# Optimization experiments

Hardware: AMD Instinct MI355X
Metric: run time of the kernel (lower is better)

## Reference

```python
import jax, jax.numpy as jnp
import numpy as np
import math

D_MODEL = 2048
HEADS = 16
D_K = D_MODEL // HEADS  # 128
D_FF = 2048
N = 8192
EPS = 1e-6


def _norm(x, alpha, bias):
    # torch Norm: alpha * (x - mean) / (std + eps) + bias, std uses ddof=1
    mu = jnp.mean(x, axis=-1, keepdims=True)
    sd = jnp.std(x, axis=-1, ddof=1, keepdims=True)
    return alpha * (x - mu) / (sd + EPS) + bias


def setup_inputs() -> dict:
    key = jax.random.key(0)
    ks = jax.random.split(key, 16)
    s = 0.02
    inp = {
        "q": jax.random.normal(ks[0], (N, D_MODEL), jnp.float32),
        "k": jax.random.normal(ks[1], (N, D_MODEL), jnp.float32),
        "v": jax.random.normal(ks[2], (N, D_MODEL), jnp.float32),
        # norm params (norm_1 exists in module but is unused in forward)
        "nq_a": jnp.ones((D_MODEL,), jnp.float32), "nq_b": jnp.zeros((D_MODEL,), jnp.float32),
        "nk_a": jnp.ones((D_MODEL,), jnp.float32), "nk_b": jnp.zeros((D_MODEL,), jnp.float32),
        "nv_a": jnp.ones((D_MODEL,), jnp.float32), "nv_b": jnp.zeros((D_MODEL,), jnp.float32),
        "n2_a": jnp.ones((D_MODEL,), jnp.float32), "n2_b": jnp.zeros((D_MODEL,), jnp.float32),
        # attention projections, stored [in, out]
        "Wq": jax.random.normal(ks[3], (D_MODEL, D_MODEL), jnp.float32) * s,
        "bq": jnp.zeros((D_MODEL,), jnp.float32),
        "Wk": jax.random.normal(ks[4], (D_MODEL, D_MODEL), jnp.float32) * s,
        "bk": jnp.zeros((D_MODEL,), jnp.float32),
        "Wv": jax.random.normal(ks[5], (D_MODEL, D_MODEL), jnp.float32) * s,
        "bv": jnp.zeros((D_MODEL,), jnp.float32),
        "Wo": jax.random.normal(ks[6], (D_MODEL, D_MODEL), jnp.float32) * s,
        "bo": jnp.zeros((D_MODEL,), jnp.float32),
        # FFN
        "W1": jax.random.normal(ks[7], (D_MODEL, D_FF), jnp.float32) * s,
        "b1": jnp.zeros((D_FF,), jnp.float32),
        "W2": jax.random.normal(ks[8], (D_FF, D_MODEL), jnp.float32) * s,
        "b2": jnp.zeros((D_MODEL,), jnp.float32),
    }
    return inp


def reference(q, k, v,
              nq_a, nq_b, nk_a, nk_b, nv_a, nv_b, n2_a, n2_b,
              Wq, bq, Wk, bk, Wv, bv, Wo, bo, W1, b1, W2, b2):
    x = v  # residual stream (dropout is identity at inference)
    qn = _norm(q, nq_a, nq_b)
    kn = _norm(k, nk_a, nk_b)
    vn = _norm(v, nv_a, nv_b)

    # projections -> [N, h, d_k] then transpose(1,2) -> [N, d_k, h]
    qh = (qn @ Wq + bq).reshape(N, HEADS, D_K).transpose(0, 2, 1)
    kh = (kn @ Wk + bk).reshape(N, HEADS, D_K).transpose(0, 2, 1)
    vh = (vn @ Wv + bv).reshape(N, HEADS, D_K).transpose(0, 2, 1)

    # NON-STANDARD (as-written in source): per-token [d_k, d_k] attention
    # contracting over the head axis, scaled by 1/sqrt(d_k).
    scores = jnp.einsum('nah,nbh->nab', qh, kh) / math.sqrt(D_K)  # [N, d_k, d_k]
    probs = jax.nn.softmax(scores, axis=-1)
    attn = jnp.einsum('nab,nbh->nah', probs, vh)  # [N, d_k, h]

    concat = attn.transpose(0, 2, 1).reshape(N, D_MODEL)  # [N, h*d_k]
    x = x + (concat @ Wo + bo)

    x2 = _norm(x, n2_a, n2_b)
    ff = jax.nn.relu(x2 @ W1 + b1) @ W2 + b2
    return x + ff
```

## Files before the change

### kernel.cpp

```cpp
#include <hip/hip_runtime.h>
#include <hip/hip_bf16.h>

#define DM 2048
#define NTOK 8192
#define EPS 1e-6f

typedef __attribute__((ext_vector_type(8))) short short8;
typedef __attribute__((ext_vector_type(4))) short short4v;
typedef __attribute__((ext_vector_type(4))) float f32x4;
typedef __attribute__((ext_vector_type(16))) float f32x16;
typedef __attribute__((ext_vector_type(4))) unsigned int u32x4;

typedef const __attribute__((address_space(1))) void gvoid;
typedef __attribute__((address_space(3))) void lvoid;

static __device__ __forceinline__ unsigned short f2bf(float f) {
    unsigned u = __builtin_bit_cast(unsigned, f);
    unsigned r = u + 0x7FFFu + ((u >> 16) & 1u);
    return (unsigned short)(r >> 16);
}
static __device__ __forceinline__ float bf2f(unsigned short h) {
    return __builtin_bit_cast(float, (unsigned)h << 16);
}

__global__ __launch_bounds__(256) void norm_rows(
        const float* __restrict__ in, const float* __restrict__ alpha,
        const float* __restrict__ beta, unsigned short* __restrict__ out) {
    const int row = blockIdx.x;
    const int t = threadIdx.x;
    const float* x = in + (size_t)row * DM + t * 8;
    float4 v0 = *(const float4*)(x);
    float4 v1 = *(const float4*)(x + 4);
    float s = (v0.x + v0.y) + (v0.z + v0.w) + (v1.x + v1.y) + (v1.z + v1.w);
    float ss = v0.x*v0.x + v0.y*v0.y + v0.z*v0.z + v0.w*v0.w
             + v1.x*v1.x + v1.y*v1.y + v1.z*v1.z + v1.w*v1.w;
    #pragma unroll
    for (int m = 1; m < 64; m <<= 1) {
        s  += __shfl_xor(s, m);
        ss += __shfl_xor(ss, m);
    }
    __shared__ float red[8];
    const int wv = t >> 6, ln = t & 63;
    if (ln == 0) { red[wv] = s; red[4 + wv] = ss; }
    __syncthreads();
    s  = (red[0] + red[1]) + (red[2] + red[3]);
    ss = (red[4] + red[5]) + (red[6] + red[7]);
    const float mu = s * (1.0f / DM);
    float var = (ss - s * mu) * (1.0f / (DM - 1));
    var = fmaxf(var, 0.0f);
    const float scale = 1.0f / (sqrtf(var) + EPS);
    float4 a0 = *(const float4*)(alpha + t*8);
    float4 a1 = *(const float4*)(alpha + t*8 + 4);
    float4 b0 = *(const float4*)(beta + t*8);
    float4 b1 = *(const float4*)(beta + t*8 + 4);
    short8 o;
    o[0] = (short)f2bf(a0.x * (v0.x - mu) * scale + b0.x);
    o[1] = (short)f2bf(a0.y * (v0.y - mu) * scale + b0.y);
    o[2] = (short)f2bf(a0.z * (v0.z - mu) * scale + b0.z);
    o[3] = (short)f2bf(a0.w * (v0.w - mu) * scale + b0.w);
    o[4] = (short)f2bf(a1.x * (v1.x - mu) * scale + b1.x);
    o[5] = (short)f2bf(a1.y * (v1.y - mu) * scale + b1.y);
    o[6] = (short)f2bf(a1.z * (v1.z - mu) * scale + b1.z);
    o[7] = (short)f2bf(a1.w * (v1.w - mu) * scale + b1.w);
    *(short8*)(out + (size_t)row * DM + t * 8) = o;
}

__global__ __launch_bounds__(256) void norm_rows_bf16(
        const unsigned short* __restrict__ in, const float* __restrict__ alpha,
        const float* __restrict__ beta, unsigned short* __restrict__ out) {
    const int row = blockIdx.x;
    const int t = threadIdx.x;
    short8 rv = *(const short8*)(in + (size_t)row * DM + t * 8);
    float xv[8];
    #pragma unroll
    for (int j = 0; j < 8; ++j) xv[j] = bf2f((unsigned short)rv[j]);
    float s = 0.f, ss = 0.f;
    #pragma unroll
    for (int j = 0; j < 8; ++j) { s += xv[j]; ss += xv[j]*xv[j]; }
    #pragma unroll
    for (int m = 1; m < 64; m <<= 1) {
        s  += __shfl_xor(s, m);
        ss += __shfl_xor(ss, m);
    }
    __shared__ float red[8];
    const int wv = t >> 6, ln = t & 63;
    if (ln == 0) { red[wv] = s; red[4 + wv] = ss; }
    __syncthreads();
    s  = (red[0] + red[1]) + (red[2] + red[3]);
    ss = (red[4] + red[5]) + (red[6] + red[7]);
    const float mu = s * (1.0f / DM);
    float var = (ss - s * mu) * (1.0f / (DM - 1));
    var = fmaxf(var, 0.0f);
    const float scale = 1.0f / (sqrtf(var) + EPS);
    short8 o;
    #pragma unroll
    for (int j = 0; j < 8; ++j) {
        const float av = alpha[t*8 + j], bv = beta[t*8 + j];
        o[j] = (short)f2bf(av * (xv[j] - mu) * scale + bv);
    }
    *(short8*)(out + (size_t)row * DM + t * 8) = o;
}

__global__ __launch_bounds__(256) void wtrans6(
        const float* __restrict__ Wq, const float* __restrict__ Wk,
        const float* __restrict__ Wv, const float* __restrict__ Wo,
        const float* __restrict__ W1, const float* __restrict__ W2,
        unsigned short* __restrict__ Tq, unsigned short* __restrict__ Tk,
        unsigned short* __restrict__ Tv, unsigned short* __restrict__ To,
        unsigned short* __restrict__ T1, unsigned short* __restrict__ T2,
        float isq) {
    __shared__ float tile[32][33];
    const int z = blockIdx.z;
    const float* W = z==0?Wq: z==1?Wk: z==2?Wv: z==3?Wo: z==4?W1: W2;
    unsigned short* Wt = z==0?Tq: z==1?Tk: z==2?Tv: z==3?To: z==4?T1: T2;
    const int perm = (z < 2) ? 1 : 0;
    const float ws = (z == 0) ? isq : 1.0f;
    const int bc = blockIdx.x * 32, bk = blockIdx.y * 32;
    const int t = threadIdx.x;
    const int tc = t & 31, tr = t >> 5;
    #pragma unroll
    for (int i = 0; i < 4; ++i)
        tile[tr + i*8][tc] = W[(size_t)(bk + tr + i*8) * DM + bc + tc];
    __syncthreads();
    #pragma unroll
    for (int i = 0; i < 4; ++i) {
        const int c = bc + tr + i*8;
        const int pc = perm ? ((c & 127) * 16 + (c >> 7)) : c;
        Wt[(size_t)pc * DM + bk + tc] = f2bf(tile[tc][tr + i*8] * ws);
    }
}

#define BARRIER __builtin_amdgcn_s_barrier()
#define WAIT_LGKM0 asm volatile("s_waitcnt lgkmcnt(0)" ::: "memory")
#define VMCNT(n) asm volatile("s_waitcnt vmcnt(" #n ")" ::: "memory")

template<int EPI>
__global__ __launch_bounds__(512, 2) void gemm256(
        const unsigned short* __restrict__ A, const unsigned short* __restrict__ Bt,
        const float* __restrict__ bias, const float* __restrict__ residF,
        const unsigned short* __restrict__ residB,
        float* __restrict__ outF, unsigned short* __restrict__ outB, int biasPerm,
        float bscale) {
    __shared__ __align__(16) char lds[131072];
    char* ldsA = lds;
    char* ldsB = lds + 65536;

    const int t = threadIdx.x, l = t & 63, w = t >> 6;
    const int wm = w >> 2, wn = w & 3;

    const int b = blockIdx.x;
    const int xcd = b & 7;
    const int j = b >> 3;
    const int m0 = (xcd * 4 + (j & 3)) * 256;
    const int n0 = (j >> 2) * 256;

    const int rS = t >> 3;
    const int cS = ((t & 7) ^ (rS & 7)) * 8;
    const unsigned short* aSt = A  + (size_t)(m0 + rS) * 2048 + cS;
    const unsigned short* bSt = Bt + (size_t)(n0 + rS) * 2048 + cS;
    const int ldsStW = w * 1024;

    const int aRd = wm * 16384 + (l & 15) * 128;
    const int bRd = (wn >> 1) * 16384 + (wn & 1) * 8192 + (l & 15) * 128;
    const int ch0 = (((l >> 4) + 0) ^ (l & 7)) * 16;
    const int ch1 = (((l >> 4) + 4) ^ (l & 7)) * 16;

    short8 af[8][2], bf[4][2];
    f32x4 acc[8][4] = {};

#define STG_A(buf, h, kt) do { \
    __builtin_amdgcn_global_load_lds((gvoid*)(aSt + (size_t)((h)*128)*2048 + (kt)*64), \
        (lvoid*)(ldsA + (buf)*32768 + (h)*16384 + ldsStW), 16, 0, 0); \
    __builtin_amdgcn_global_load_lds((gvoid*)(aSt + (size_t)((h)*128+64)*2048 + (kt)*64), \
        (lvoid*)(ldsA + (buf)*32768 + (h)*16384 + 8192 + ldsStW), 16, 0, 0); \
} while(0)
#define STG_B(buf, h, kt) do { \
    __builtin_amdgcn_global_load_lds((gvoid*)(bSt + (size_t)((h)*128)*2048 + (kt)*64), \
        (lvoid*)(ldsB + (buf)*32768 + (h)*16384 + ldsStW), 16, 0, 0); \
    __builtin_amdgcn_global_load_lds((gvoid*)(bSt + (size_t)((h)*128+64)*2048 + (kt)*64), \
        (lvoid*)(ldsB + (buf)*32768 + (h)*16384 + 8192 + ldsStW), 16, 0, 0); \
} while(0)
#define RD_A(buf, mh) do { \
    _Pragma("unroll") for (int ml = 0; ml < 4; ++ml) { \
        af[(mh)*4+ml][0] = *(const short8*)(ldsA + (buf)*32768 + aRd + ((mh)*4+ml)*2048 + ch0); \
        af[(mh)*4+ml][1] = *(const short8*)(ldsA + (buf)*32768 + aRd + ((mh)*4+ml)*2048 + ch1); \
    } } while(0)
#define RD_B(buf, nh) do { \
    _Pragma("unroll") for (int nl = 0; nl < 2; ++nl) { \
        bf[(nh)*2+nl][0] = *(const short8*)(ldsB + (buf)*32768 + bRd + ((nh)*2+nl)*2048 + ch0); \
        bf[(nh)*2+nl][1] = *(const short8*)(ldsB + (buf)*32768 + bRd + ((nh)*2+nl)*2048 + ch1); \
    } } while(0)
#define MM_Q(mh, nh) do { \
    _Pragma("unroll") for (int ml = 0; ml < 4; ++ml) \
    _Pragma("unroll") for (int nl = 0; nl < 2; ++nl) { \
        acc[(mh)*4+ml][(nh)*2+nl] = __builtin_amdgcn_mfma_f32_16x16x32_bf16( \
            af[(mh)*4+ml][0], bf[(nh)*2+nl][0], acc[(mh)*4+ml][(nh)*2+nl], 0, 0, 0); \
        acc[(mh)*4+ml][(nh)*2+nl] = __builtin_amdgcn_mfma_f32_16x16x32_bf16( \
            af[(mh)*4+ml][1], bf[(nh)*2+nl][1], acc[(mh)*4+ml][(nh)*2+nl], 0, 0, 0); \
    } \
} while(0)

    STG_A(0, 0, 0); STG_A(0, 1, 0);
    STG_B(0, 0, 0); STG_B(0, 1, 0);
    STG_A(1, 0, 1); STG_A(1, 1, 1);
    VMCNT(4);
    BARRIER;

    #pragma unroll 1
    for (int i = 0; i < 16; ++i) {
        const int kt1 = 2*i + 1, k2 = 2*i + 2, k3 = 2*i + 3;
        const bool more = (i < 15);
        RD_A(0, 0); RD_A(0, 1); RD_B(0, 0);
        STG_B(1, 0, kt1); STG_B(1, 1, kt1);
        BARRIER; WAIT_LGKM0;
        __builtin_amdgcn_s_setprio(1);
        MM_Q(0, 0); MM_Q(1, 0);
        __builtin_amdgcn_s_setprio(0);
        BARRIER;
        RD_B(0, 1);
        if (more) { STG_A(0, 0, k2); STG_A(0, 1, k2); VMCNT(4); } else { VMCNT(0); }
        BARRIER; WAIT_LGKM0;
        __builtin_amdgcn_s_setprio(1);
        MM_Q(0, 1); MM_Q(1, 1);
        __builtin_amdgcn_s_setprio(0);
        BARRIER;
        RD_A(1, 0); RD_A(1, 1); RD_B(1, 0);
        if (more) { STG_B(0, 0, k2); STG_B(0, 1, k2); }
        BARRIER; WAIT_LGKM0;
        __builtin_amdgcn_s_setprio(1);
        MM_Q(0, 0); MM_Q(1, 0);
        __builtin_amdgcn_s_setprio(0);
        BARRIER;
        RD_B(1, 1);
        if (more) { STG_A(1, 0, k3); STG_A(1, 1, k3); VMCNT(4); }
        BARRIER; WAIT_LGKM0;
        __builtin_amdgcn_s_setprio(1);
        MM_Q(0, 1); MM_Q(1, 1);
        __builtin_amdgcn_s_setprio(0);
        BARRIER;
    }

    unsigned short* cs = (unsigned short*)lds;
    #pragma unroll 1
    for (int pass = 0; pass < 2; ++pass) {
        BARRIER;
        if (wm == pass) {
            #pragma unroll
            for (int ni = 0; ni < 4; ++ni) {
                const int col = wn*64 + ni*16 + (l & 15);
                const int gcol = n0 + col;
                const int cb = biasPerm ? ((gcol >> 4) + (gcol & 15) * 128) : gcol;
                const float bvv = bias[cb] * bscale;
                #pragma unroll
                for (int mi = 0; mi < 8; ++mi) {
                    #pragma unroll
                    for (int r = 0; r < 4; ++r) {
                        const int row = mi*16 + (l >> 4)*4 + r;
                        float vv = acc[mi][ni][r] + bvv;
                        if (EPI == 1) vv = fmaxf(vv, 0.0f);
                        cs[row*260 + col] = f2bf(vv);
                    }
                }
            }
        }
        BARRIER;
        #pragma unroll
        for (int s = 0; s < 8; ++s) {
            const int row = (t >> 5) + s*16;
            const int seg = t & 31;
            short8 pk = *(const short8*)(cs + row*260 + seg*8);
            const int grow = m0 + pass*128 + row;
            const size_t gb = (size_t)grow * 2048 + n0 + seg*8;
            if (EPI == 3) {
                float4 r0 = *(const float4*)(residF + gb);
                float4 r1 = *(const float4*)(residF + gb + 4);
                short8 o;
                o[0] = (short)f2bf(bf2f((unsigned short)pk[0]) + r0.x);
                o[1] = (short)f2bf(bf2f((unsigned short)pk[1]) + r0.y);
                o[2] = (short)f2bf(bf2f((unsigned short)pk[2]) + r0.z);
                o[3] = (short)f2bf(bf2f((unsigned short)pk[3]) + r0.w);
                o[4] = (short)f2bf(bf2f((unsigned short)pk[4]) + r1.x);
                o[5] = (short)f2bf(bf2f((unsigned short)pk[5]) + r1.y);
                o[6] = (short)f2bf(bf2f((unsigned short)pk[6]) + r1.z);
                o[7] = (short)f2bf(bf2f((unsigned short)pk[7]) + r1.w);
                *(short8*)(outB + gb) = o;
            } else if (EPI == 4) {
                short8 rb = *(const short8*)(residB + gb);
                float4 o0, o1;
                o0.x = bf2f((unsigned short)pk[0]) + bf2f((unsigned short)rb[0]);
                o0.y = bf2f((unsigned short)pk[1]) + bf2f((unsigned short)rb[1]);
                o0.z = bf2f((unsigned short)pk[2]) + bf2f((unsigned short)rb[2]);
                o0.w = bf2f((unsigned short)pk[3]) + bf2f((unsigned short)rb[3]);
                o1.x = bf2f((unsigned short)pk[4]) + bf2f((unsigned short)rb[4]);
                o1.y = bf2f((unsigned short)pk[5]) + bf2f((unsigned short)rb[5]);
                o1.z = bf2f((unsigned short)pk[6]) + bf2f((unsigned short)rb[6]);
                o1.w = bf2f((unsigned short)pk[7]) + bf2f((unsigned short)rb[7]);
                *(float4*)(outF + gb) = o0;
                *(float4*)(outF + gb + 4) = o1;
            } else {
                *(short8*)(outB + gb) = pk;
            }
        }
    }
#undef STG_A
#undef STG_B
#undef RD_A
#undef RD_B
#undef MM_Q
}

__global__ __launch_bounds__(256) void attn_tok(
        const unsigned short* __restrict__ Qt, const unsigned short* __restrict__ Kt,
        const unsigned short* __restrict__ Vp, unsigned short* __restrict__ Cc) {
    const int n = blockIdx.x;
    const int t = threadIdx.x, w = t >> 6, l = t & 63;
    const int q31 = l & 31, hi = l >> 5;
    __shared__ __align__(16) unsigned short c_s[16 * 132];

    const size_t tb = (size_t)n * DM;
    const short8 qf = *(const short8*)(Qt + tb + (w*32 + q31)*16 + hi*8);
    short8 kf[4];
    #pragma unroll
    for (int bt = 0; bt < 4; ++bt)
        kf[bt] = *(const short8*)(Kt + tb + (bt*32 + q31)*16 + hi*8);
    short8 vf[8];
    #pragma unroll
    for (int ks = 0; ks < 8; ++ks)
        vf[ks] = *(const short8*)(Vp + tb + (q31 & 15)*128 + ks*16 + hi*8);

    const f32x16 z = {};
    f32x16 sc[4];
    #pragma unroll
    for (int bt = 0; bt < 4; ++bt)
        sc[bt] = __builtin_amdgcn_mfma_f32_32x32x16_bf16(kf[bt], qf, z, 0, 0, 0);

    float m0 = sc[0][0], m1 = sc[1][0], m2 = sc[2][0], m3 = sc[3][0];
    #pragma unroll
    for (int r = 1; r < 16; ++r) {
        m0 = fmaxf(m0, sc[0][r]); m1 = fmaxf(m1, sc[1][r]);
        m2 = fmaxf(m2, sc[2][r]); m3 = fmaxf(m3, sc[3][r]);
    }
    float mx = fmaxf(fmaxf(m0, m1), fmaxf(m2, m3));
    { float a2 = mx, b2 = mx;
      asm volatile("v_permlane32_swap_b32 %0, %1" : "+v"(a2), "+v"(b2));
      mx = fmaxf(a2, b2); }

    float p[4][16];
    float s0 = 0.f, s1 = 0.f, s2 = 0.f, s3 = 0.f;
    #pragma unroll
    for (int r = 0; r < 16; ++r) {
        p[0][r] = __expf(sc[0][r] - mx); s0 += p[0][r];
        p[1][r] = __expf(sc[1][r] - mx); s1 += p[1][r];
        p[2][r] = __expf(sc[2][r] - mx); s2 += p[2][r];
        p[3][r] = __expf(sc[3][r] - mx); s3 += p[3][r];
    }
    float sm = (s0 + s1) + (s2 + s3);
    { float a2 = sm, b2 = sm;
      asm volatile("v_permlane32_swap_b32 %0, %1" : "+v"(a2), "+v"(b2));
      sm = a2 + b2; }
    const float inv = __builtin_amdgcn_rcpf(sm);
    #pragma unroll
    for (int bt = 0; bt < 4; ++bt)
        #pragma unroll
        for (int r = 0; r < 16; ++r)
            p[bt][r] *= inv;

    f32x16 acc = {};
    #pragma unroll
    for (int ks = 0; ks < 8; ++ks) {
        const int bt = ks >> 1, r0 = (ks & 1) * 8;
        unsigned X0, Y0, X1, Y1;
        asm("v_cvt_pk_bf16_f32 %0, %1, %2" : "=v"(X0) : "v"(p[bt][r0+0]), "v"(p[bt][r0+1]));
        asm("v_cvt_pk_bf16_f32 %0, %1, %2" : "=v"(Y0) : "v"(p[bt][r0+4]), "v"(p[bt][r0+5]));
        asm("v_cvt_pk_bf16_f32 %0, %1, %2" : "=v"(X1) : "v"(p[bt][r0+2]), "v"(p[bt][r0+3]));
        asm("v_cvt_pk_bf16_f32 %0, %1, %2" : "=v"(Y1) : "v"(p[bt][r0+6]), "v"(p[bt][r0+7]));
        asm volatile("v_permlane32_swap_b32 %0, %1" : "+v"(X0), "+v"(Y0));
        asm volatile("v_permlane32_swap_b32 %0, %1" : "+v"(X1), "+v"(Y1));
        u32x4 pw; pw[0] = X0; pw[1] = X1; pw[2] = Y0; pw[3] = Y1;
        const short8 paf = __builtin_bit_cast(short8, pw);
        acc = __builtin_amdgcn_mfma_f32_32x32x16_bf16(paf, vf[ks], acc, 0, 0, 0);
    }

    if (q31 < 16) {
        #pragma unroll
        for (int rp = 0; rp < 8; ++rp) {
            const int r = rp * 2;
            const int a = (r & 3) + 8 * (r >> 2) + 4 * hi;
            unsigned pk;
            asm("v_cvt_pk_bf16_f32 %0, %1, %2" : "=v"(pk) : "v"(acc[r]), "v"(acc[r+1]));
            *(unsigned*)((char*)c_s + q31*264 + (w*32 + a)*2) = pk;
        }
    }
    __syncthreads();
    *(short8*)(Cc + tb + t*8) = *(const short8*)((char*)c_s + (t >> 4)*264 + (t & 15)*16);
}

extern "C" void kernel_launch(void* const* d_in, const int* in_sizes, int n_in,
                              void* d_out, int out_size, void* d_ws, size_t ws_size,
                              hipStream_t stream) {
    (void)in_sizes; (void)n_in; (void)out_size; (void)ws_size;
    const float* q    = (const float*)d_in[0];
    const float* k    = (const float*)d_in[1];
    const float* v    = (const float*)d_in[2];
    const float* nq_a = (const float*)d_in[3];
    const float* nq_b = (const float*)d_in[4];
    const float* nk_a = (const float*)d_in[5];
    const float* nk_b = (const float*)d_in[6];
    const float* nv_a = (const float*)d_in[7];
    const float* nv_b = (const float*)d_in[8];
    const float* n2_a = (const float*)d_in[9];
    const float* n2_b = (const float*)d_in[10];
    const float* Wq   = (const float*)d_in[11];
    const float* bq   = (const float*)d_in[12];
    const float* Wk   = (const float*)d_in[13];
    const float* bk   = (const float*)d_in[14];
    const float* Wv   = (const float*)d_in[15];
    const float* bv   = (const float*)d_in[16];
    const float* Wo   = (const float*)d_in[17];
    const float* bo   = (const float*)d_in[18];
    const float* W1   = (const float*)d_in[19];
    const float* b1   = (const float*)d_in[20];
    const float* W2   = (const float*)d_in[21];
    const float* b2   = (const float*)d_in[22];

    char* ws = (char*)d_ws;
    const size_t MB = 1024 * 1024;
    unsigned short* buf0 = (unsigned short*)(ws);
    unsigned short* QtB  = (unsigned short*)(ws + 32*MB);
    unsigned short* KtB  = (unsigned short*)(ws + 64*MB);
    unsigned short* VpB  = (unsigned short*)(ws + 96*MB);
    unsigned short* Wqt  = (unsigned short*)(ws + 128*MB);
    unsigned short* Wkt  = (unsigned short*)(ws + 136*MB);
    unsigned short* Wvt  = (unsigned short*)(ws + 144*MB);
    unsigned short* Wot  = (unsigned short*)(ws + 152*MB);
    unsigned short* W1t  = (unsigned short*)(ws + 160*MB);
    unsigned short* W2t  = (unsigned short*)(ws + 168*MB);
    unsigned short* x2   = QtB;
    unsigned short* h1   = KtB;
    unsigned short* xb   = VpB;
    float* x = (float*)d_out;

    const float isq = 0.088388347648318447f;

    dim3 b256(256);
    dim3 gT6(DM / 32, DM / 32, 6);
    wtrans6<<<gT6, b256, 0, stream>>>(Wq, Wk, Wv, Wo, W1, W2,
                                      Wqt, Wkt, Wvt, Wot, W1t, W2t, isq);

    dim3 gN(NTOK);
    dim3 gG(256);
    dim3 b512(512);

    norm_rows<<<gN, b256, 0, stream>>>(q, nq_a, nq_b, buf0);
    gemm256<0><<<gG, b512, 0, stream>>>(buf0, Wqt, bq, nullptr, nullptr, nullptr, QtB, 1, isq);
    norm_rows<<<gN, b256, 0, stream>>>(k, nk_a, nk_b, buf0);
    gemm256<0><<<gG, b512, 0, stream>>>(buf0, Wkt, bk, nullptr, nullptr, nullptr, KtB, 1, 1.0f);
    norm_rows<<<gN, b256, 0, stream>>>(v, nv_a, nv_b, buf0);
    gemm256<0><<<gG, b512, 0, stream>>>(buf0, Wvt, bv, nullptr, nullptr, nullptr, VpB, 0, 1.0f);
    attn_tok<<<gN, b256, 0, stream>>>(QtB, KtB, VpB, buf0);
    gemm256<3><<<gG, b512, 0, stream>>>(buf0, Wot, bo, v, nullptr, nullptr, xb, 0, 1.0f);
    norm_rows_bf16<<<gN, b256, 0, stream>>>(xb, n2_a, n2_b, x2);
    gemm256<1><<<gG, b512, 0, stream>>>(x2, W1t, b1, nullptr, nullptr, nullptr, h1, 0, 1.0f);
    gemm256<4><<<gG, b512, 0, stream>>>(h1, W2t, b2, nullptr, xb, x, nullptr, 0, 1.0f);
}
```

Baseline: 559.8 us.

## Restructure GEMM main loop into per-k-tile step with fewer barriers

Replaces the four-phase ping-pong schedule, which had eight barriers and explicit lgkm waits per two k-tiles, with a simpler per-k-tile step. Each step reads its LDS fragments interleaved with MFMAs, then issues the global-to-LDS loads for tile k+2 into the same buffer, with two barriers. The goal is to cut barrier and wait overhead and let the compiler overlap LDS reads with MFMA. In exchange, global prefetch is issued only after compute on the buffer finishes, so load latency may be less hidden. LDS read waits are left to the compiler.

```diff
diff --git a/kernel.cpp b/kernel.cpp
--- a/kernel.cpp
+++ b/kernel.cpp
@@ -131,7 +131,6 @@
 }
 
 #define BARRIER __builtin_amdgcn_s_barrier()
-#define WAIT_LGKM0 asm volatile("s_waitcnt lgkmcnt(0)" ::: "memory")
 #define VMCNT(n) asm volatile("s_waitcnt vmcnt(" #n ")" ::: "memory")
 
 template<int EPI>
@@ -200,44 +199,36 @@
     } \
 } while(0)
 
-    STG_A(0, 0, 0); STG_A(0, 1, 0);
-    STG_B(0, 0, 0); STG_B(0, 1, 0);
-    STG_A(1, 0, 1); STG_A(1, 1, 1);
-    VMCNT(4);
+#define KSTEP(c, kt) do { \
+    RD_A(c, 0); RD_B(c, 0); \
+    __builtin_amdgcn_s_setprio(1); \
+    MM_Q(0, 0); \
+    RD_B(c, 1); \
+    MM_Q(0, 1); \
+    RD_A(c, 1); \
+    MM_Q(1, 1); \
+    MM_Q(1, 0); \
+    __builtin_amdgcn_s_setprio(0); \
+    BARRIER; \
+    if ((kt) + 2 < 32) { \
+        STG_A(c, 0, (kt)+2); STG_A(c, 1, (kt)+2); \
+        STG_B(c, 0, (kt)+2); STG_B(c, 1, (kt)+2); \
+        VMCNT(8); \
+    } else { \
+        VMCNT(0); \
+    } \
+    BARRIER; \
+} while(0)
+
+    STG_A(0, 0, 0); STG_A(0, 1, 0); STG_B(0, 0, 0); STG_B(0, 1, 0);
+    STG_A(1, 0, 1); STG_A(1, 1, 1); STG_B(1, 0, 1); STG_B(1, 1, 1);
+    VMCNT(8);
     BARRIER;
 
     #pragma unroll 1
     for (int i = 0; i < 16; ++i) {
-        const int kt1 = 2*i + 1, k2 = 2*i + 2, k3 = 2*i + 3;
-        const bool more = (i < 15);
-        RD_A(0, 0); RD_A(0, 1); RD_B(0, 0);
-        STG_B(1, 0, kt1); STG_B(1, 1, kt1);
-        BARRIER; WAIT_LGKM0;
-        __builtin_amdgcn_s_setprio(1);
-        MM_Q(0, 0); MM_Q(1, 0);
-        __builtin_amdgcn_s_setprio(0);
-        BARRIER;
-        RD_B(0, 1);
-        if (more) { STG_A(0, 0, k2); STG_A(0, 1, k2); VMCNT(4); } else { VMCNT(0); }
-        BARRIER; WAIT_LGKM0;
-        __builtin_amdgcn_s_setprio(1);
-        MM_Q(0, 1); MM_Q(1, 1);
-        __builtin_amdgcn_s_setprio(0);
-        BARRIER;
-        RD_A(1, 0); RD_A(1, 1); RD_B(1, 0);
-        if (more) { STG_B(0, 0, k2); STG_B(0, 1, k2); }
-        BARRIER; WAIT_LGKM0;
-        __builtin_amdgcn_s_setprio(1);
-        MM_Q(0, 0); MM_Q(1, 0);
-        __builtin_amdgcn_s_setprio(0);
-        BARRIER;
-        RD_B(1, 1);
-        if (more) { STG_A(1, 0, k3); STG_A(1, 1, k3); VMCNT(4); }
-        BARRIER; WAIT_LGKM0;
-        __builtin_amdgcn_s_setprio(1);
-        MM_Q(0, 1); MM_Q(1, 1);
-        __builtin_amdgcn_s_setprio(0);
-        BARRIER;
+        KSTEP(0, 2*i);
+        KSTEP(1, 2*i + 1);
     }
 
     unsigned short* cs = (unsigned short*)lds;
@@ -302,6 +293,7 @@
             }
         }
     }
+#undef KSTEP
 #undef STG_A
 #undef STG_B
 #undef RD_A
```

New measurement: 566.6 us. About the same (+1.2%).
